# Optimization experiments

Hardware: AMD Instinct MI355X
Metric: run time of the kernel (lower is better)

Reference implementation:

```python
import jax, jax.numpy as jnp
import numpy as np

# YOLOv4 stride-8 head config (yolov4.cfg)
ALL_ANCHORS = [[12,16],[19,36],[40,28],[36,75],[76,55],[72,146],[142,110],[192,243],[459,401]]
ANCHOR_MASK = [0, 1, 2]
N_CLASSES = 80
SCALE_XY = 1.2  # scale_x_y for this head
N_BBOX_ATTRS = 5  # tx, ty, tw, th, obj


def setup_inputs() -> dict:
    key = jax.random.key(0)
    attrs = N_CLASSES + N_BBOX_ATTRS  # 85
    n_anchors = len(ANCHOR_MASK)      # 3
    # raw conv output: [batch, n_anchors*attrs, grid, grid]
    x = jax.random.normal(key, (16, n_anchors * attrs, 76, 76), dtype=jnp.float32)
    return {"x": x, "input_dim": 608}


def reference(x, input_dim):
    B = x.shape[0]
    G = x.shape[2]                      # grid_dim (INPUT_H_DIM)
    stride = input_dim // G             # grid_stride
    A = len(ANCHOR_MASK)
    attrs = N_CLASSES + N_BBOX_ATTRS

    # anchors scaled to grid units: [A, 2]
    anc = jnp.asarray([ALL_ANCHORS[i] for i in ANCHOR_MASK], dtype=jnp.float32) / stride

    # [B, A, attrs, H, W] -> [B, H, W, A, attrs]
    x = x.reshape(B, A, attrs, G, G).transpose(0, 3, 4, 1, 2)

    # yolo_transform: sigmoid+scale tx/ty, exp*anchor tw/th, sigmoid obj+cls
    txy = jax.nn.sigmoid(x[..., 0:2]) * SCALE_XY - (SCALE_XY - 1.0) / 2.0
    twh = jnp.exp(x[..., 2:4]) * anc            # broadcast over [B,H,W,A,2]
    objcls = jax.nn.sigmoid(x[..., 4:])

    # add_grid_offsets: torch.meshgrid(grid, grid) is 'ij' -> y_offset[i,j]=i, x_offset[i,j]=j
    gy, gx = jnp.meshgrid(jnp.arange(G), jnp.arange(G), indexing="ij")
    off = jnp.stack([gx, gy], axis=-1).astype(jnp.float32)[:, :, None, :]  # [H,W,1,2]
    txy = txy + off

    # scale bbox attrs (tx..th) to input-image pixels
    boxes = jnp.concatenate([txy, twh], axis=-1) * jnp.float32(stride)

    out = jnp.concatenate([boxes, objcls], axis=-1)  # [B,H,W,A,attrs]
    return out.reshape(B, G * G * A, attrs)
```

## Files before the change

kernel.cpp:

```cpp
#include <hip/hip_runtime.h>

#define GRIDD  76
#define NROWS  255
#define GG     (GRIDD * GRIDD)
#define HROWS  64
#define UPITCH 76
#define UDW    (2 * HROWS * UPITCH)

typedef __attribute__((address_space(3))) unsigned lds_u32;
typedef __attribute__((address_space(1))) unsigned glb_u32;

__device__ __forceinline__ void gll16(const float* g, float* l) {
    __builtin_amdgcn_global_load_lds((const glb_u32*)g, (lds_u32*)l, 16, 0, 0);
}

__device__ __forceinline__ void stage_half(const float* __restrict__ src,
                                           float* dstbase,
                                           unsigned wid, unsigned lane)
{
    #pragma unroll
    for (unsigned k = 0; k < 2u; ++k) {
        unsigned i   = k * 512u + (wid << 6) + lane;
        unsigned row = i / 19u;
        unsigned qc  = i - row * 19u;
        gll16(src + (size_t)row * GG + (qc << 2),
              dstbase + (size_t)(k * 512u + (wid << 6)) * 4u);
    }
    {
        unsigned i = 1024u + wid * 24u + lane;
        if (lane < 24u) {
            unsigned row = i / 19u;
            unsigned qc  = i - row * 19u;
            gll16(src + (size_t)row * GG + (qc << 2),
                  dstbase + (size_t)(1024u + wid * 24u) * 4u);
        }
    }
}

__device__ __forceinline__ void compute_half(const float* __restrict__ bc,
                                             float* __restrict__ outbh,
                                             unsigned remBase, unsigned lane,
                                             unsigned wid, float stride, float fh)
{
    const unsigned rem  = remBase + lane;
    const unsigned a    = (rem >= 170u) ? 2u : ((rem >= 85u) ? 1u : 0u);
    const unsigned attr = rem - a * 85u;
    const bool  wh  = (attr == 2u) | (attr == 3u);
    const bool  isx = (attr == 0u);
    float anc = 0.f;
    if (attr == 2u) anc = (a == 0u) ? 12.f : ((a == 1u) ? 19.f : 40.f);
    if (attr == 3u) anc = (a == 0u) ? 16.f : ((a == 1u) ? 36.f : 28.f);
    const float mB    = -0.1f * stride;
    const float slog  = wh ? 1.44269504f : -1.44269504f;
    const float A2    = wh ? anc : ((attr < 2u) ? 1.2f * stride : 1.f);
    const float wsel  = isx ? stride : 0.f;
    const float basef = (attr == 1u) ? fmaf(fh, stride, mB) : (isx ? mB : 0.f);
    float* __restrict__ dst = outbh + rem;

    #pragma unroll
    for (unsigned j = 0; j < 3u; ++j) {
        const unsigned tt = wid + (j << 3);
        if (tt < 19u) {
            const float4 vv = *reinterpret_cast<const float4*>(
                bc + (size_t)lane * UPITCH + (tt << 2));
            #pragma unroll
            for (unsigned i = 0; i < 4u; ++i) {
                const float v  = (i == 0) ? vv.x : (i == 1) ? vv.y : (i == 2) ? vv.z : vv.w;
                const float uf = (float)((tt << 2) + i);
                const float e2 = exp2f(v * slog);
                const float sg = __builtin_amdgcn_rcpf(1.0f + e2);
                const float q  = wh ? e2 : sg;
                const float o  = fmaf(q, A2, fmaf(uf, wsel, basef));
                dst[(size_t)((tt << 2) + i) * NROWS] = o;
            }
        }
    }
}

__global__ __launch_bounds__(512, 8) void yolo_head_kernel(
    const float* __restrict__ x, const int* __restrict__ dimp,
    float* __restrict__ out)
{
    __shared__ float buf[UDW];
    const unsigned lb    = (blockIdx.x & 7u) * 304u + (blockIdx.x >> 3);
    const unsigned b     = lb / 152u;
    const unsigned hr    = lb - b * 152u;
    const unsigned h     = hr >> 1;
    const unsigned rbase = (hr & 1u) * 127u;
    const unsigned t     = threadIdx.x;
    const unsigned wid   = t >> 6;
    const unsigned lane  = t & 63u;
    const float stride   = (float)(*dimp / GRIDD);
    const float fh       = (float)h;

    const float* __restrict__ src0 = x + (size_t)(b * NROWS + rbase) * GG + h * GRIDD;
    stage_half(src0,                        buf,                  wid, lane);
    stage_half(src0 + (size_t)HROWS * GG,   buf + HROWS * UPITCH, wid, lane);

    asm volatile("s_waitcnt vmcnt(3)\n\ts_barrier" ::: "memory");

    float* __restrict__ outbh = out + (size_t)(b * GRIDD + h) * (GRIDD * NROWS);
    compute_half(buf, outbh, rbase, lane, wid, stride, fh);

    __syncthreads();
    compute_half(buf + HROWS * UPITCH, outbh, rbase + HROWS, lane, wid, stride, fh);
}

extern "C" void kernel_launch(void* const* d_in, const int* in_sizes, int n_in,
                              void* d_out, int out_size, void* d_ws, size_t ws_size,
                              hipStream_t stream) {
    const float* x  = (const float*)d_in[0];
    const int* dimp = (const int*)d_in[1];
    float* out      = (float*)d_out;
    const int B = in_sizes[0] / (NROWS * GG);
    yolo_head_kernel<<<B * GRIDD * 2, 512, 0, stream>>>(x, dimp, out);
}
```

Before: 37.56 us.

## Split each grid row into four 64-row quarter blocks of 256 threads

Each block now stages and transforms a 64-channel quarter of one grid row, where it used to process two 64-row halves. The grid grows to four blocks per row with 256 threads and half the LDS per block. This drops the in-block two-phase pipeline (partial waitcnt overlap of the second half's loads with the first half's compute) in favour of more, smaller blocks for latency hiding. The last quarter starts at row 191, so its channels overlap the third quarter and one channel is written twice with the same value.

```diff
diff --git a/kernel.cpp b/kernel.cpp
--- a/kernel.cpp
+++ b/kernel.cpp
@@ -3,9 +3,9 @@
 #define GRIDD  76
 #define NROWS  255
 #define GG     (GRIDD * GRIDD)
-#define HROWS  64
-#define UPITCH 76
-#define UDW    (2 * HROWS * UPITCH)
+#define QROWS  64
+#define QQ     (QROWS * 19)
+#define QDW    (QROWS * GRIDD)
 
 typedef __attribute__((address_space(3))) unsigned lds_u32;
 typedef __attribute__((address_space(1))) unsigned glb_u32;
@@ -14,35 +14,37 @@
     __builtin_amdgcn_global_load_lds((const glb_u32*)g, (lds_u32*)l, 16, 0, 0);
 }
 
-__device__ __forceinline__ void stage_half(const float* __restrict__ src,
-                                           float* dstbase,
-                                           unsigned wid, unsigned lane)
+__global__ __launch_bounds__(256, 8) void yolo_head_kernel(
+    const float* __restrict__ x, const int* __restrict__ dimp,
+    float* __restrict__ out)
 {
+    __shared__ float buf[QDW];
+    const unsigned lb    = (blockIdx.x & 7u) * 608u + (blockIdx.x >> 3);
+    const unsigned b     = lb / 304u;
+    const unsigned hq    = lb - b * 304u;
+    const unsigned h     = hq >> 2;
+    const unsigned q     = hq & 3u;
+    const unsigned rbase = (q == 3u) ? 191u : (q << 6);
+    const unsigned t     = threadIdx.x;
+    const unsigned wid   = t >> 6;
+    const unsigned lane  = t & 63u;
+    const float stride   = (float)(*dimp / GRIDD);
+    const float fh       = (float)h;
+
+    const float* __restrict__ src = x + (size_t)(b * NROWS + rbase) * GG + h * GRIDD;
     #pragma unroll
-    for (unsigned k = 0; k < 2u; ++k) {
-        unsigned i   = k * 512u + (wid << 6) + lane;
-        unsigned row = i / 19u;
-        unsigned qc  = i - row * 19u;
-        gll16(src + (size_t)row * GG + (qc << 2),
-              dstbase + (size_t)(k * 512u + (wid << 6)) * 4u);
-    }
-    {
-        unsigned i = 1024u + wid * 24u + lane;
-        if (lane < 24u) {
+    for (unsigned k = 0; k < 5u; ++k) {
+        unsigned i = k * 256u + (wid << 6) + lane;
+        if (i < QQ) {
             unsigned row = i / 19u;
             unsigned qc  = i - row * 19u;
             gll16(src + (size_t)row * GG + (qc << 2),
-                  dstbase + (size_t)(1024u + wid * 24u) * 4u);
+                  buf + (size_t)(k * 256u + (wid << 6)) * 4u);
         }
     }
-}
+    __syncthreads();
 
-__device__ __forceinline__ void compute_half(const float* __restrict__ bc,
-                                             float* __restrict__ outbh,
-                                             unsigned remBase, unsigned lane,
-                                             unsigned wid, float stride, float fh)
-{
-    const unsigned rem  = remBase + lane;
+    const unsigned rem  = rbase + lane;
     const unsigned a    = (rem >= 170u) ? 2u : ((rem >= 85u) ? 1u : 0u);
     const unsigned attr = rem - a * 85u;
     const bool  wh  = (attr == 2u) | (attr == 3u);
@@ -55,55 +57,26 @@
     const float A2    = wh ? anc : ((attr < 2u) ? 1.2f * stride : 1.f);
     const float wsel  = isx ? stride : 0.f;
     const float basef = (attr == 1u) ? fmaf(fh, stride, mB) : (isx ? mB : 0.f);
-    float* __restrict__ dst = outbh + rem;
+    float* __restrict__ dst = out + (size_t)(b * GRIDD + h) * (GRIDD * NROWS) + rem;
 
     #pragma unroll
-    for (unsigned j = 0; j < 3u; ++j) {
-        const unsigned tt = wid + (j << 3);
+    for (unsigned j = 0; j < 5u; ++j) {
+        const unsigned tt = wid + (j << 2);
         if (tt < 19u) {
             const float4 vv = *reinterpret_cast<const float4*>(
-                bc + (size_t)lane * UPITCH + (tt << 2));
+                buf + (size_t)lane * GRIDD + (tt << 2));
             #pragma unroll
             for (unsigned i = 0; i < 4u; ++i) {
                 const float v  = (i == 0) ? vv.x : (i == 1) ? vv.y : (i == 2) ? vv.z : vv.w;
                 const float uf = (float)((tt << 2) + i);
                 const float e2 = exp2f(v * slog);
                 const float sg = __builtin_amdgcn_rcpf(1.0f + e2);
-                const float q  = wh ? e2 : sg;
-                const float o  = fmaf(q, A2, fmaf(uf, wsel, basef));
+                const float qv = wh ? e2 : sg;
+                const float o  = fmaf(qv, A2, fmaf(uf, wsel, basef));
                 dst[(size_t)((tt << 2) + i) * NROWS] = o;
             }
         }
     }
-}
-
-__global__ __launch_bounds__(512, 8) void yolo_head_kernel(
-    const float* __restrict__ x, const int* __restrict__ dimp,
-    float* __restrict__ out)
-{
-    __shared__ float buf[UDW];
-    const unsigned lb    = (blockIdx.x & 7u) * 304u + (blockIdx.x >> 3);
-    const unsigned b     = lb / 152u;
-    const unsigned hr    = lb - b * 152u;
-    const unsigned h     = hr >> 1;
-    const unsigned rbase = (hr & 1u) * 127u;
-    const unsigned t     = threadIdx.x;
-    const unsigned wid   = t >> 6;
-    const unsigned lane  = t & 63u;
-    const float stride   = (float)(*dimp / GRIDD);
-    const float fh       = (float)h;
-
-    const float* __restrict__ src0 = x + (size_t)(b * NROWS + rbase) * GG + h * GRIDD;
-    stage_half(src0,                        buf,                  wid, lane);
-    stage_half(src0 + (size_t)HROWS * GG,   buf + HROWS * UPITCH, wid, lane);
-
-    asm volatile("s_waitcnt vmcnt(3)\n\ts_barrier" ::: "memory");
-
-    float* __restrict__ outbh = out + (size_t)(b * GRIDD + h) * (GRIDD * NROWS);
-    compute_half(buf, outbh, rbase, lane, wid, stride, fh);
-
-    __syncthreads();
-    compute_half(buf + HROWS * UPITCH, outbh, rbase + HROWS, lane, wid, stride, fh);
 }
 
 extern "C" void kernel_launch(void* const* d_in, const int* in_sizes, int n_in,
@@ -113,5 +86,5 @@
     const int* dimp = (const int*)d_in[1];
     float* out      = (float*)d_out;
     const int B = in_sizes[0] / (NROWS * GG);
-    yolo_head_kernel<<<B * GRIDD * 2, 512, 0, stream>>>(x, dimp, out);
+    yolo_head_kernel<<<B * GRIDD * 4, 256, 0, stream>>>(x, dimp, out);
 }
```

Result: faster. 32.96 us (-12.3%).
